# Kernel optimization log

Hardware: AMD Instinct MI355X
Metric: run time of the kernel (lower is better)

Reference implementation:

```python
import jax, jax.numpy as jnp
import numpy as np

N_NODES = 100000
N_EDGES = 3200000
N_GRAPHS = 4096
BN_EPS = 1e-5


def setup_inputs() -> dict:
    key = jax.random.key(0)
    ks = iter(jax.random.split(key, 64))
    d = {}
    d["x"] = jax.random.normal(next(ks), (N_NODES, 36), dtype=jnp.float32)
    d["edge_index"] = jax.random.randint(next(ks), (2, N_EDGES), 0, N_NODES, dtype=jnp.int32)
    d["batch"] = jnp.sort(jax.random.randint(next(ks), (N_NODES,), 0, N_GRAPHS, dtype=jnp.int32))
    d["num_graphs"] = N_GRAPHS
    # GCN layers: (in, out) per hidden_dims=[128,128,64]
    dims = [(36, 128), (128, 128), (128, 64)]
    for i, (di, do) in enumerate(dims):
        d[f"w{i}"] = jax.random.normal(next(ks), (di, do), dtype=jnp.float32) * (1.0 / np.sqrt(di))
        d[f"b{i}"] = jax.random.normal(next(ks), (do,), dtype=jnp.float32) * 0.01
        d[f"g{i}"] = jax.random.uniform(next(ks), (do,), dtype=jnp.float32, minval=0.5, maxval=1.5)
        d[f"be{i}"] = jax.random.normal(next(ks), (do,), dtype=jnp.float32) * 0.01
        d[f"m{i}"] = jax.random.normal(next(ks), (do,), dtype=jnp.float32) * 0.01
        d[f"v{i}"] = jax.random.uniform(next(ks), (do,), dtype=jnp.float32, minval=0.5, maxval=1.5)
    # FC head: 64 -> 128 -> 64 -> 2
    d["fw0"] = jax.random.normal(next(ks), (64, 128), dtype=jnp.float32) * (1.0 / 8.0)
    d["fb0"] = jax.random.normal(next(ks), (128,), dtype=jnp.float32) * 0.01
    d["fw1"] = jax.random.normal(next(ks), (128, 64), dtype=jnp.float32) * (1.0 / np.sqrt(128))
    d["fb1"] = jax.random.normal(next(ks), (64,), dtype=jnp.float32) * 0.01
    d["ow"] = jax.random.normal(next(ks), (64, 2), dtype=jnp.float32) * (1.0 / 8.0)
    d["ob"] = jax.random.normal(next(ks), (2,), dtype=jnp.float32) * 0.01
    return d


def _gcn_layer(x, w, b, src, dst, norm_e, norm_self, n_nodes):
    # PyG GCNConv with self-loops: out[i] = sum_j norm_ij * (x_j @ W) + b
    xw = x @ w                                   # [N, out]
    msg = xw[src] * norm_e[:, None]              # gather + scale, [E, out]
    agg = jax.ops.segment_sum(msg, dst, num_segments=n_nodes)
    return agg + xw * norm_self[:, None] + b     # self-loop contribution + bias


def _bn_eval(x, g, be, m, v):
    return g * (x - m) * jax.lax.rsqrt(v + BN_EPS) + be


def reference(x, edge_index, batch, num_graphs,
              w0, b0, g0, be0, m0, v0,
              w1, b1, g1, be1, m1, v1,
              w2, b2, g2, be2, m2, v2,
              fw0, fb0, fw1, fb1, ow, ob):
    n = x.shape[0]
    src, dst = edge_index[0], edge_index[1]
    # symmetric GCN normalization with self-loops (gcn_norm)
    deg = jax.ops.segment_sum(jnp.ones(src.shape[0], x.dtype), dst, num_segments=n) + 1.0
    dinv = jax.lax.rsqrt(deg)
    norm_e = dinv[src] * dinv[dst]   # per-edge coeff
    norm_self = dinv * dinv          # self-loop coeff = 1/deg

    params = [(w0, b0, g0, be0, m0, v0), (w1, b1, g1, be1, m1, v1), (w2, b2, g2, be2, m2, v2)]
    h = x
    for (w, b, g, be, m, v) in params:
        h = _gcn_layer(h, w, b, src, dst, norm_e, norm_self, n)
        h = jax.nn.relu(_bn_eval(h, g, be, m, v))  # dropout inactive in eval

    # global mean pool over graphs
    sums = jax.ops.segment_sum(h, batch, num_segments=num_graphs)          # [G, 64]
    cnt = jax.ops.segment_sum(jnp.ones(n, h.dtype), batch, num_segments=num_graphs)
    pooled = sums / jnp.maximum(cnt, 1.0)[:, None]

    h = jax.nn.relu(pooled @ fw0 + fb0)
    h = jax.nn.relu(h @ fw1 + fb1)
    return h @ ow + ob
```

## Files before the change

kernel.cpp:

```cpp
#include <hip/hip_runtime.h>
#include <hip/hip_fp16.h>

#define BN_EPS 1e-5f

#define BUCK_SHIFT 9
#define NBUCK_MAX 256
#define BCAP 20480
#define PBLK 512

__global__ __launch_bounds__(256) void fused_scatter(const int* __restrict__ src,
                                                     const int* __restrict__ dst,
                                                     int* __restrict__ gcnt,
                                                     int2* __restrict__ ebuf,
                                                     int nE, int nbuck, int chunk) {
    __shared__ int h[NBUCK_MAX], rbase[NBUCK_MAX], cur[NBUCK_MAX];
    const int blk = blockIdx.x, tid = threadIdx.x;
    for (int j = tid; j < nbuck; j += 256) { h[j] = 0; cur[j] = 0; }
    __syncthreads();
    const int base = blk * chunk;
    const int end = min(base + chunk, nE);
    for (int i = base + tid; i < end; i += 256)
        atomicAdd(&h[dst[i] >> BUCK_SHIFT], 1);
    __syncthreads();
    for (int j = tid; j < nbuck; j += 256)
        rbase[j] = h[j] ? atomicAdd(&gcnt[j], h[j]) : 0;
    __syncthreads();
    for (int i = base + tid; i < end; i += 256) {
        int s = src[i], d = dst[i];
        int b = d >> BUCK_SHIFT;
        int p = rbase[b] + atomicAdd(&cur[b], 1);
        if (p < BCAP) ebuf[(size_t)b * BCAP + p] = make_int2(s, d);
    }
}

__global__ __launch_bounds__(256) void fused_csr(const int2* __restrict__ ebuf,
                                                 const int* __restrict__ gcnt,
                                                 const float* __restrict__ x,
                                                 const int* __restrict__ batch,
                                                 int* __restrict__ degI,
                                                 float* __restrict__ dinv,
                                                 int* __restrict__ row_start,
                                                 int* __restrict__ src_sorted,
                                                 __half* __restrict__ xs_h,
                                                 float* __restrict__ cnt, int n) {
    __shared__ int deg[512];
    __shared__ int cur[512];
    __shared__ float sdi[512];
    __shared__ int tmp[256];
    __shared__ int s_low_total;
    const int b = blockIdx.x, tid = threadIdx.x;
    const int nb = b << BUCK_SHIFT;
    const int cntb = min(gcnt[b], BCAP);
    const int2* __restrict__ eb = ebuf + (size_t)b * BCAP;

    for (int j = tid; j < 512; j += 256) deg[j] = 0;
    __syncthreads();
    for (int i = tid; i < cntb; i += 256)
        atomicAdd(&deg[eb[i].y - nb], 1);
    __syncthreads();

    for (int j = tid; j < 512; j += 256) {
        int node = nb + j;
        if (node < n) {
            int d = deg[j];
            degI[node] = d;
            float di = rsqrtf((float)d + 1.0f);
            dinv[node] = di;
            sdi[j] = di;
        }
    }

    int v0 = deg[tid];
    tmp[tid] = v0;
    __syncthreads();
    for (int off = 1; off < 256; off <<= 1) {
        int t = (tid >= off) ? tmp[tid - off] : 0;
        __syncthreads();
        tmp[tid] += t;
        __syncthreads();
    }
    int ex_low = tmp[tid] - v0;
    if (tid == 255) s_low_total = tmp[255];
    __syncthreads();
    int low_total = s_low_total;
    int v1 = deg[256 + tid];
    __syncthreads();
    tmp[tid] = v1;
    __syncthreads();
    for (int off = 1; off < 256; off <<= 1) {
        int t = (tid >= off) ? tmp[tid - off] : 0;
        __syncthreads();
        tmp[tid] += t;
        __syncthreads();
    }
    int ex_high = tmp[tid] - v1 + low_total;

    const int gbase = b * BCAP;
    if (nb + tid < n) row_start[nb + tid] = gbase + ex_low;
    if (nb + 256 + tid < n) row_start[nb + 256 + tid] = gbase + ex_high;
    cur[tid] = ex_low;
    cur[256 + tid] = ex_high;
    __syncthreads();

    for (int i = tid; i < cntb; i += 256) {
        int2 ed = eb[i];
        int p = atomicAdd(&cur[ed.y - nb], 1);
        src_sorted[gbase + p] = ed.x;
    }

    for (int idx = tid; idx < 512 * 18; idx += 256) {
        int j = idx / 18;
        int node = nb + j;
        if (node < n) {
            int c = idx - j * 18;
            float2 v = *(const float2*)(x + (size_t)node * 36 + 2 * c);
            float di = sdi[j];
            *(__half2*)(xs_h + (size_t)node * 36 + 2 * c) = __floats2half2_rn(v.x * di, v.y * di);
        }
    }

    for (int j = tid; j < 512; j += 256) {
        int node = nb + j;
        if (node < n) unsafeAtomicAdd(&cnt[batch[node]], 1.0f);
    }
}

__global__ __launch_bounds__(256) void agg_pull36w_h(const __half* __restrict__ xs_h,
                                                     const int* __restrict__ row_start,
                                                     const int* __restrict__ degI,
                                                     const int* __restrict__ src_sorted,
                                                     const float* __restrict__ dinv,
                                                     __half* __restrict__ out, int n) {
    int node = __builtin_amdgcn_readfirstlane((int)(blockIdx.x * 4 + (threadIdx.x >> 6)));
    if (node >= n) return;
    const int lane = threadIdx.x & 63;
    int e = row_start[node];
    const int re = e + degI[node];
    const float di = dinv[node];

    const char* __restrict__ xb = (const char*)xs_h;
    const unsigned loff = (unsigned)lane << 2;

    float2 acc = make_float2(0.f, 0.f);
    if (lane < 18) acc = __half22float2(*(const __half2*)(xb + ((unsigned)node * 72u + loff)));

    for (; e + 3 < re; e += 4) {
        int s0 = src_sorted[e], s1 = src_sorted[e + 1],
            s2 = src_sorted[e + 2], s3 = src_sorted[e + 3];
        if (lane < 18) {
            float2 a0 = __half22float2(*(const __half2*)(xb + ((unsigned)s0 * 72u + loff)));
            float2 a1 = __half22float2(*(const __half2*)(xb + ((unsigned)s1 * 72u + loff)));
            float2 a2 = __half22float2(*(const __half2*)(xb + ((unsigned)s2 * 72u + loff)));
            float2 a3 = __half22float2(*(const __half2*)(xb + ((unsigned)s3 * 72u + loff)));
            acc.x += (a0.x + a1.x) + (a2.x + a3.x);
            acc.y += (a0.y + a1.y) + (a2.y + a3.y);
        }
    }
    for (; e < re; e++) {
        int s = src_sorted[e];
        if (lane < 18) {
            float2 a = __half22float2(*(const __half2*)(xb + ((unsigned)s * 72u + loff)));
            acc.x += a.x;
            acc.y += a.y;
        }
    }
    if (lane < 18) {
        __half2 o = __floats2half2_rn(acc.x * di, acc.y * di);
        *(__half2*)((char*)out + ((unsigned)node * 72u + loff)) = o;
    }
}

__global__ __launch_bounds__(256) void agg_pull_wave2_h(const __half* __restrict__ feat_h,
                                                        const int* __restrict__ row_start,
                                                        const int* __restrict__ degI,
                                                        const int* __restrict__ src_sorted,
                                                        const float* __restrict__ dinv,
                                                        __half* __restrict__ out, int n) {
    int node = __builtin_amdgcn_readfirstlane((int)(blockIdx.x * 4 + (threadIdx.x >> 6)));
    if (node >= n) return;
    const int lane = threadIdx.x & 63;
    int e = row_start[node];
    const int re = e + degI[node];
    const float di = dinv[node];

    const char* __restrict__ fb = (const char*)feat_h;
    const unsigned loff = (unsigned)lane << 2;

    float2 acc = __half22float2(*(const __half2*)(fb + (((unsigned)node << 8) + loff)));

    for (; e + 3 < re; e += 4) {
        int s0 = src_sorted[e], s1 = src_sorted[e + 1],
            s2 = src_sorted[e + 2], s3 = src_sorted[e + 3];
        float2 a0 = __half22float2(*(const __half2*)(fb + (((unsigned)s0 << 8) + loff)));
        float2 a1 = __half22float2(*(const __half2*)(fb + (((unsigned)s1 << 8) + loff)));
        float2 a2 = __half22float2(*(const __half2*)(fb + (((unsigned)s2 << 8) + loff)));
        float2 a3 = __half22float2(*(const __half2*)(fb + (((unsigned)s3 << 8) + loff)));
        acc.x += (a0.x + a1.x) + (a2.x + a3.x);
        acc.y += (a0.y + a1.y) + (a2.y + a3.y);
    }
    for (; e < re; e++) {
        int s = src_sorted[e];
        float2 a = __half22float2(*(const __half2*)(fb + (((unsigned)s << 8) + loff)));
        acc.x += a.x;
        acc.y += a.y;
    }
    __half2 o = __floats2half2_rn(acc.x * di, acc.y * di);
    *(__half2*)((char*)out + (((unsigned)node << 8) + loff)) = o;
}

template<int IN, int OUT, bool BNRELU, bool SCALEOUT>
__global__ __launch_bounds__(256) void gemm_rth(const __half* __restrict__ in,
                                                const float* __restrict__ W,
                                                const float* __restrict__ bias,
                                                const float* __restrict__ gg,
                                                const float* __restrict__ bb,
                                                const float* __restrict__ mm,
                                                const float* __restrict__ vv,
                                                const float* __restrict__ dscale,
                                                __half* __restrict__ out, int n) {
    constexpr int BM = 64;
    constexpr int TN = 8;
    constexpr int CG = OUT / TN;
    constexpr int RG = 256 / CG;
    constexpr int TM = BM / RG;
    constexpr int PAD = (IN == 36) ? 8 : 4;
    constexpr int LDW = IN + PAD;
    __shared__ float s_a[BM][LDW];

    const int r0 = blockIdx.x * BM;
    const int tid = threadIdx.x;

    if constexpr (IN == 128) {
        for (int i8 = tid; i8 < BM * 16; i8 += 256) {
            int idx = i8 * 8;
            int r = idx >> 7;
            int k = idx & 127;
            int row = r0 + r;
            uint4 v = make_uint4(0u, 0u, 0u, 0u);
            if (row < n) v = *(const uint4*)(in + (size_t)row * 128 + k);
            const __half2* hp = (const __half2*)&v;
            float2 f0 = __half22float2(hp[0]);
            float2 f1 = __half22float2(hp[1]);
            float2 f2 = __half22float2(hp[2]);
            float2 f3 = __half22float2(hp[3]);
            *(float4*)&s_a[r][k]     = make_float4(f0.x, f0.y, f1.x, f1.y);
            *(float4*)&s_a[r][k + 4] = make_float4(f2.x, f2.y, f3.x, f3.y);
        }
    } else {
        for (int i2 = tid; i2 < BM * (IN / 2); i2 += 256) {
            int r = i2 / (IN / 2);
            int k = (i2 - r * (IN / 2)) * 2;
            int row = r0 + r;
            __half2 hv;
            *(unsigned*)&hv = 0u;
            if (row < n) hv = *(const __half2*)(in + (size_t)row * IN + k);
            float2 f = __half22float2(hv);
            s_a[r][k] = f.x;
            s_a[r][k + 1] = f.y;
        }
    }
    __syncthreads();

    const int tx = tid % CG;
    const int ty = tid / CG;
    const int c0 = tx * TN;
    const int rr = ty * TM;

    float acc[TM][TN];
#pragma unroll
    for (int j = 0; j < TM; j++)
#pragma unroll
        for (int t = 0; t < TN; t++) acc[j][t] = 0.0f;

#pragma unroll 2
    for (int k = 0; k < IN; k += 4) {
        float4 a[TM];
#pragma unroll
        for (int j = 0; j < TM; j++) a[j] = *(const float4*)&s_a[rr + j][k];
#pragma unroll
        for (int kk = 0; kk < 4; kk++) {
            float4 wv0 = *(const float4*)(W + (size_t)(k + kk) * OUT + c0);
            float4 wv1 = *(const float4*)(W + (size_t)(k + kk) * OUT + c0 + 4);
#pragma unroll
            for (int j = 0; j < TM; j++) {
                float av = (kk == 0) ? a[j].x : (kk == 1) ? a[j].y : (kk == 2) ? a[j].z : a[j].w;
                acc[j][0] += av * wv0.x;
                acc[j][1] += av * wv0.y;
                acc[j][2] += av * wv0.z;
                acc[j][3] += av * wv0.w;
                acc[j][4] += av * wv1.x;
                acc[j][5] += av * wv1.y;
                acc[j][6] += av * wv1.z;
                acc[j][7] += av * wv1.w;
            }
        }
    }

    float scl[TN], sft[TN];
    if constexpr (BNRELU) {
#pragma unroll
        for (int t = 0; t < TN; t++) {
            float s = gg[c0 + t] * rsqrtf(vv[c0 + t] + BN_EPS);
            scl[t] = s;
            sft[t] = bb[c0 + t] + (bias[c0 + t] - mm[c0 + t]) * s;
        }
    }

#pragma unroll
    for (int j = 0; j < TM; j++) {
        int row = r0 + rr + j;
        if (row < n) {
            float ds = 1.0f;
            if constexpr (SCALEOUT) ds = dscale[row];
            union { __half h[8]; uint4 v; } u;
#pragma unroll
            for (int t = 0; t < TN; t++) {
                float val = acc[j][t];
                if constexpr (BNRELU) val = fmaxf(val * scl[t] + sft[t], 0.0f);
                if constexpr (SCALEOUT) val *= ds;
                u.h[t] = __float2half_rn(val);
            }
            *(uint4*)(out + (size_t)row * OUT + c0) = u.v;
        }
    }
}

__global__ __launch_bounds__(256) void agg_pull_pool_h(const __half* __restrict__ feat_h,
                                                       const int* __restrict__ row_start,
                                                       const int* __restrict__ degI,
                                                       const int* __restrict__ src_sorted,
                                                       const float* __restrict__ dinv,
                                                       const float* __restrict__ bias,
                                                       const float* __restrict__ gg,
                                                       const float* __restrict__ bb,
                                                       const float* __restrict__ mm,
                                                       const float* __restrict__ vv,
                                                       const int* __restrict__ batch,
                                                       float* __restrict__ pool, int n) {
    int node = __builtin_amdgcn_readfirstlane((int)(blockIdx.x * 4 + (threadIdx.x >> 6)));
    if (node >= n) return;
    const int lane = threadIdx.x & 63;
    int e = row_start[node];
    const int re = e + degI[node];
    const float di = dinv[node];

    const char* __restrict__ fb = (const char*)feat_h;
    const unsigned loff = (unsigned)lane << 1;

    float acc = __half2float(*(const __half*)(fb + (((unsigned)node << 7) + loff)));

    for (; e + 3 < re; e += 4) {
        int s0 = src_sorted[e], s1 = src_sorted[e + 1],
            s2 = src_sorted[e + 2], s3 = src_sorted[e + 3];
        float a0 = __half2float(*(const __half*)(fb + (((unsigned)s0 << 7) + loff)));
        float a1 = __half2float(*(const __half*)(fb + (((unsigned)s1 << 7) + loff)));
        float a2 = __half2float(*(const __half*)(fb + (((unsigned)s2 << 7) + loff)));
        float a3 = __half2float(*(const __half*)(fb + (((unsigned)s3 << 7) + loff)));
        acc += (a0 + a1) + (a2 + a3);
    }
    for (; e < re; e++) {
        acc += __half2float(*(const __half*)(fb + (((unsigned)src_sorted[e] << 7) + loff)));
    }
    float h = acc * di + bias[lane];
    float scale = gg[lane] * rsqrtf(vv[lane] + BN_EPS);
    float val = fmaxf((h - mm[lane]) * scale + bb[lane], 0.0f);
    unsafeAtomicAdd(&pool[(size_t)batch[node] * 64 + lane], val);
}

__global__ __launch_bounds__(128) void fc_head_kernel(const float* __restrict__ pool,
                                                      const float* __restrict__ cnt,
                                                      const float* __restrict__ fw0,
                                                      const float* __restrict__ fb0,
                                                      const float* __restrict__ fw1,
                                                      const float* __restrict__ fb1,
                                                      const float* __restrict__ ow,
                                                      const float* __restrict__ ob,
                                                      float* __restrict__ out) {
    int g = blockIdx.x, tid = threadIdx.x;
    __shared__ float p[64], h1[128], h2[64];
    if (tid < 64) p[tid] = pool[g * 64 + tid] / fmaxf(cnt[g], 1.0f);
    __syncthreads();
    {
        float acc = fb0[tid];
        for (int k = 0; k < 64; k++) acc += p[k] * fw0[k * 128 + tid];
        h1[tid] = fmaxf(acc, 0.0f);
    }
    __syncthreads();
    if (tid < 64) {
        float acc = fb1[tid];
        for (int k = 0; k < 128; k++) acc += h1[k] * fw1[k * 64 + tid];
        h2[tid] = fmaxf(acc, 0.0f);
    }
    __syncthreads();
    if (tid < 2) {
        float acc = ob[tid];
        for (int k = 0; k < 64; k++) acc += h2[k] * ow[k * 2 + tid];
        out[g * 2 + tid] = acc;
    }
}

extern "C" void kernel_launch(void* const* d_in, const int* in_sizes, int n_in,
                              void* d_out, int out_size, void* d_ws, size_t ws_size,
                              hipStream_t stream) {
    const float* x     = (const float*)d_in[0];
    const int*   eidx  = (const int*)d_in[1];
    const int*   batch = (const int*)d_in[2];
    const float* w0 = (const float*)d_in[4];
    const float* b0 = (const float*)d_in[5];
    const float* g0 = (const float*)d_in[6];
    const float* be0 = (const float*)d_in[7];
    const float* m0 = (const float*)d_in[8];
    const float* v0 = (const float*)d_in[9];
    const float* w1 = (const float*)d_in[10];
    const float* b1 = (const float*)d_in[11];
    const float* g1 = (const float*)d_in[12];
    const float* be1 = (const float*)d_in[13];
    const float* m1 = (const float*)d_in[14];
    const float* v1 = (const float*)d_in[15];
    const float* w2 = (const float*)d_in[16];
    const float* b2 = (const float*)d_in[17];
    const float* g2 = (const float*)d_in[18];
    const float* be2 = (const float*)d_in[19];
    const float* m2 = (const float*)d_in[20];
    const float* v2 = (const float*)d_in[21];
    const float* fw0 = (const float*)d_in[22];
    const float* fb0 = (const float*)d_in[23];
    const float* fw1 = (const float*)d_in[24];
    const float* fb1 = (const float*)d_in[25];
    const float* ow = (const float*)d_in[26];
    const float* ob = (const float*)d_in[27];

    const int N = in_sizes[0] / 36;
    const int E = in_sizes[1] / 2;
    const int G = out_size / 2;
    const int* src = eidx;
    const int* dst = eidx + E;

    const int nbuck = (N + 511) >> BUCK_SHIFT;
    const int chunk = (E + PBLK - 1) / PBLK;

    char* wsb = (char*)d_ws;
    int2*   ebuf       = (int2*)wsb;    wsb += (size_t)nbuck * BCAP * 8;
    __half* F1         = (__half*)wsb;  wsb += (size_t)N * 128 * 2;
    __half* F1a        = (__half*)wsb;  wsb += (size_t)N * 128 * 2;
    __half* F2         = (__half*)wsb;  wsb += (size_t)N * 64 * 2;
    __half* A36h       = (__half*)wsb;  wsb += (size_t)N * 36 * 2;
    __half* xs_h       = (__half*)wsb;  wsb += (size_t)N * 36 * 2;
    int*    src_sorted = (int*)wsb;     wsb += (size_t)nbuck * BCAP * 4;
    int*    degI       = (int*)wsb;     wsb += (size_t)N * 4;
    int*    row_start  = (int*)wsb;     wsb += (size_t)N * 4;
    float*  dinv       = (float*)wsb;   wsb += (size_t)N * 4;
    float*  pool       = (float*)wsb;   wsb += (size_t)G * 64 * 4;
    float*  cnt        = (float*)wsb;   wsb += (size_t)G * 4;
    int*    gcnt       = (int*)wsb;     wsb += 256 * 4;
    __half* F1b        = (__half*)ebuf;

    hipMemsetAsync(gcnt, 0, 256 * 4, stream);
    hipMemsetAsync(pool, 0, (size_t)G * 64 * 4, stream);
    hipMemsetAsync(cnt, 0, (size_t)G * 4, stream);

    fused_scatter<<<PBLK, 256, 0, stream>>>(src, dst, gcnt, ebuf, E, nbuck, chunk);
    fused_csr<<<nbuck, 256, 0, stream>>>(ebuf, gcnt, x, batch, degI, dinv, row_start,
                                         src_sorted, xs_h, cnt, N);

    const int NW = (N + 3) / 4;
    const int NG = (N + 63) / 64;

    agg_pull36w_h<<<NW, 256, 0, stream>>>(xs_h, row_start, degI, src_sorted, dinv, A36h, N);
    gemm_rth<36, 128, true, true><<<NG, 256, 0, stream>>>(
        A36h, w0, b0, g0, be0, m0, v0, dinv, F1, N);

    agg_pull_wave2_h<<<NW, 256, 0, stream>>>(F1, row_start, degI, src_sorted, dinv, F1a, N);
    gemm_rth<128, 128, true, false><<<NG, 256, 0, stream>>>(
        F1a, w1, b1, g1, be1, m1, v1, nullptr, F1b, N);

    gemm_rth<128, 64, false, true><<<NG, 256, 0, stream>>>(
        F1b, w2, nullptr, nullptr, nullptr, nullptr, nullptr, dinv, F2, N);

    agg_pull_pool_h<<<NW, 256, 0, stream>>>(
        F2, row_start, degI, src_sorted, dinv, b2, g2, be2, m2, v2, batch, pool, N);

    fc_head_kernel<<<G, 128, 0, stream>>>(pool, cnt, fw0, fb0, fw1, fb1, ow, ob, (float*)d_out);
}
```

Measured before the change: 670.1 us.

## Replace scalar FP32 GEMMs with MFMA f16 kernels using repacked weights

Replaces the shared-memory scalar FMA GEMM kernels for all three GCN layers with MFMA 16x16x32 f16 kernels. Weights are converted to half and laid out per lane by a small repack kernel each call. The layer-0 aggregation output is padded from 36 to 64 columns so K fits the MFMA shape, and row buffers are padded to a multiple of 64. Weights now run in half precision, and the 36-wide path relies on the padding lanes (18..31) writing zero accumulators.

```diff
diff --git a/kernel.cpp b/kernel.cpp
--- a/kernel.cpp
+++ b/kernel.cpp
@@ -7,6 +7,9 @@
 #define NBUCK_MAX 256
 #define BCAP 20480
 #define PBLK 512
+
+typedef _Float16 f16x8 __attribute__((ext_vector_type(8)));
+typedef float f32x4 __attribute__((ext_vector_type(4)));
 
 __global__ __launch_bounds__(256) void fused_scatter(const int* __restrict__ src,
                                                      const int* __restrict__ dst,
@@ -125,6 +128,96 @@
     }
 }
 
+__global__ __launch_bounds__(256) void repack_w(const float* __restrict__ w0,
+                                                const float* __restrict__ w1,
+                                                const float* __restrict__ w2,
+                                                __half* __restrict__ Wp0,
+                                                __half* __restrict__ Wp1,
+                                                __half* __restrict__ Wp2) {
+    const int tid = threadIdx.x;
+    if (blockIdx.x == 0) {
+        for (int idx = tid; idx < 8 * 4 * 64 * 8; idx += 256) {
+            int j = idx & 7, lane = (idx >> 3) & 63, kb = (idx >> 9) & 3, nt = idx >> 11;
+            int k = kb * 32 + (lane >> 4) * 8 + j, c = nt * 16 + (lane & 15);
+            Wp1[idx] = __float2half_rn(w1[k * 128 + c]);
+        }
+    } else if (blockIdx.x == 1) {
+        for (int idx = tid; idx < 4 * 4 * 64 * 8; idx += 256) {
+            int j = idx & 7, lane = (idx >> 3) & 63, kb = (idx >> 9) & 3, nt = idx >> 11;
+            int k = kb * 32 + (lane >> 4) * 8 + j, c = nt * 16 + (lane & 15);
+            Wp2[idx] = __float2half_rn(w2[k * 64 + c]);
+        }
+    } else {
+        for (int idx = tid; idx < 8 * 2 * 64 * 8; idx += 256) {
+            int j = idx & 7, lane = (idx >> 3) & 63, kb = (idx >> 9) & 1, nt = idx >> 10;
+            int k = kb * 32 + (lane >> 4) * 8 + j, c = nt * 16 + (lane & 15);
+            Wp0[idx] = (k < 36) ? __float2half_rn(w0[k * 128 + c]) : __float2half_rn(0.0f);
+        }
+    }
+}
+
+template<int LDK, int KB, int OUT, int NT, bool BNRELU, bool SCALEOUT>
+__global__ __launch_bounds__(256) void gemm_mfma(const __half* __restrict__ in,
+                                                 const __half* __restrict__ Wp,
+                                                 const float* __restrict__ bias,
+                                                 const float* __restrict__ gg,
+                                                 const float* __restrict__ bb,
+                                                 const float* __restrict__ mm,
+                                                 const float* __restrict__ vv,
+                                                 const float* __restrict__ dscale,
+                                                 __half* __restrict__ out, int n) {
+    const int lane = threadIdx.x & 63;
+    const int wave = threadIdx.x >> 6;
+    const int r0 = blockIdx.x * 64 + wave * 16;
+    const int arow = r0 + (lane & 15);
+    const int kg = lane >> 4;
+
+    f16x8 a[KB];
+#pragma unroll
+    for (int kb = 0; kb < KB; kb++)
+        a[kb] = *(const f16x8*)(in + (size_t)arow * LDK + kb * 32 + kg * 8);
+
+    f32x4 acc[NT];
+#pragma unroll
+    for (int nt = 0; nt < NT; nt++) {
+        f32x4 z = {0.0f, 0.0f, 0.0f, 0.0f};
+        acc[nt] = z;
+    }
+
+#pragma unroll
+    for (int nt = 0; nt < NT; nt++) {
+#pragma unroll
+        for (int kb = 0; kb < KB; kb++) {
+            f16x8 b = *(const f16x8*)(Wp + ((size_t)(nt * KB + kb) * 64 + lane) * 8);
+            acc[nt] = __builtin_amdgcn_mfma_f32_16x16x32_f16(a[kb], b, acc[nt], 0, 0, 0);
+        }
+    }
+
+    const int col = lane & 15;
+    const int rbase = r0 + kg * 4;
+    float ds[4] = {1.f, 1.f, 1.f, 1.f};
+    if constexpr (SCALEOUT) {
+#pragma unroll
+        for (int r = 0; r < 4; r++) ds[r] = dscale[rbase + r];
+    }
+#pragma unroll
+    for (int nt = 0; nt < NT; nt++) {
+        const int c = nt * 16 + col;
+        float s = 1.f, t = 0.f;
+        if constexpr (BNRELU) {
+            s = gg[c] * rsqrtf(vv[c] + BN_EPS);
+            t = bb[c] + (bias[c] - mm[c]) * s;
+        }
+#pragma unroll
+        for (int r = 0; r < 4; r++) {
+            float val = acc[nt][r];
+            if constexpr (BNRELU) val = fmaxf(val * s + t, 0.0f);
+            if constexpr (SCALEOUT) val *= ds[r];
+            out[(size_t)(rbase + r) * OUT + c] = __float2half_rn(val);
+        }
+    }
+}
+
 __global__ __launch_bounds__(256) void agg_pull36w_h(const __half* __restrict__ xs_h,
                                                      const int* __restrict__ row_start,
                                                      const int* __restrict__ degI,
@@ -164,9 +257,9 @@
             acc.y += a.y;
         }
     }
-    if (lane < 18) {
+    if (lane < 32) {
         __half2 o = __floats2half2_rn(acc.x * di, acc.y * di);
-        *(__half2*)((char*)out + ((unsigned)node * 72u + loff)) = o;
+        *(__half2*)((char*)out + (((unsigned)node << 7) + loff)) = o;
     }
 }
 
@@ -206,123 +299,6 @@
     }
     __half2 o = __floats2half2_rn(acc.x * di, acc.y * di);
     *(__half2*)((char*)out + (((unsigned)node << 8) + loff)) = o;
-}
-
-template<int IN, int OUT, bool BNRELU, bool SCALEOUT>
-__global__ __launch_bounds__(256) void gemm_rth(const __half* __restrict__ in,
-                                                const float* __restrict__ W,
-                                                const float* __restrict__ bias,
-                                                const float* __restrict__ gg,
-                                                const float* __restrict__ bb,
-                                                const float* __restrict__ mm,
-                                                const float* __restrict__ vv,
-                                                const float* __restrict__ dscale,
-                                                __half* __restrict__ out, int n) {
-    constexpr int BM = 64;
-    constexpr int TN = 8;
-    constexpr int CG = OUT / TN;
-    constexpr int RG = 256 / CG;
-    constexpr int TM = BM / RG;
-    constexpr int PAD = (IN == 36) ? 8 : 4;
-    constexpr int LDW = IN + PAD;
-    __shared__ float s_a[BM][LDW];
-
-    const int r0 = blockIdx.x * BM;
-    const int tid = threadIdx.x;
-
-    if constexpr (IN == 128) {
-        for (int i8 = tid; i8 < BM * 16; i8 += 256) {
-            int idx = i8 * 8;
-            int r = idx >> 7;
-            int k = idx & 127;
-            int row = r0 + r;
-            uint4 v = make_uint4(0u, 0u, 0u, 0u);
-            if (row < n) v = *(const uint4*)(in + (size_t)row * 128 + k);
-            const __half2* hp = (const __half2*)&v;
-            float2 f0 = __half22float2(hp[0]);
-            float2 f1 = __half22float2(hp[1]);
-            float2 f2 = __half22float2(hp[2]);
-            float2 f3 = __half22float2(hp[3]);
-            *(float4*)&s_a[r][k]     = make_float4(f0.x, f0.y, f1.x, f1.y);
-            *(float4*)&s_a[r][k + 4] = make_float4(f2.x, f2.y, f3.x, f3.y);
-        }
-    } else {
-        for (int i2 = tid; i2 < BM * (IN / 2); i2 += 256) {
-            int r = i2 / (IN / 2);
-            int k = (i2 - r * (IN / 2)) * 2;
-            int row = r0 + r;
-            __half2 hv;
-            *(unsigned*)&hv = 0u;
-            if (row < n) hv = *(const __half2*)(in + (size_t)row * IN + k);
-            float2 f = __half22float2(hv);
-            s_a[r][k] = f.x;
-            s_a[r][k + 1] = f.y;
-        }
-    }
-    __syncthreads();
-
-    const int tx = tid % CG;
-    const int ty = tid / CG;
-    const int c0 = tx * TN;
-    const int rr = ty * TM;
-
-    float acc[TM][TN];
-#pragma unroll
-    for (int j = 0; j < TM; j++)
-#pragma unroll
-        for (int t = 0; t < TN; t++) acc[j][t] = 0.0f;
-
-#pragma unroll 2
-    for (int k = 0; k < IN; k += 4) {
-        float4 a[TM];
-#pragma unroll
-        for (int j = 0; j < TM; j++) a[j] = *(const float4*)&s_a[rr + j][k];
-#pragma unroll
-        for (int kk = 0; kk < 4; kk++) {
-            float4 wv0 = *(const float4*)(W + (size_t)(k + kk) * OUT + c0);
-            float4 wv1 = *(const float4*)(W + (size_t)(k + kk) * OUT + c0 + 4);
-#pragma unroll
-            for (int j = 0; j < TM; j++) {
-                float av = (kk == 0) ? a[j].x : (kk == 1) ? a[j].y : (kk == 2) ? a[j].z : a[j].w;
-                acc[j][0] += av * wv0.x;
-                acc[j][1] += av * wv0.y;
-                acc[j][2] += av * wv0.z;
-                acc[j][3] += av * wv0.w;
-                acc[j][4] += av * wv1.x;
-                acc[j][5] += av * wv1.y;
-                acc[j][6] += av * wv1.z;
-                acc[j][7] += av * wv1.w;
-            }
-        }
-    }
-
-    float scl[TN], sft[TN];
-    if constexpr (BNRELU) {
-#pragma unroll
-        for (int t = 0; t < TN; t++) {
-            float s = gg[c0 + t] * rsqrtf(vv[c0 + t] + BN_EPS);
-            scl[t] = s;
-            sft[t] = bb[c0 + t] + (bias[c0 + t] - mm[c0 + t]) * s;
-        }
-    }
-
-#pragma unroll
-    for (int j = 0; j < TM; j++) {
-        int row = r0 + rr + j;
-        if (row < n) {
-            float ds = 1.0f;
-            if constexpr (SCALEOUT) ds = dscale[row];
-            union { __half h[8]; uint4 v; } u;
-#pragma unroll
-            for (int t = 0; t < TN; t++) {
-                float val = acc[j][t];
-                if constexpr (BNRELU) val = fmaxf(val * scl[t] + sft[t], 0.0f);
-                if constexpr (SCALEOUT) val *= ds;
-                u.h[t] = __float2half_rn(val);
-            }
-            *(uint4*)(out + (size_t)row * OUT + c0) = u.v;
-        }
-    }
 }
 
 __global__ __launch_bounds__(256) void agg_pull_pool_h(const __half* __restrict__ feat_h,
@@ -438,44 +414,49 @@
 
     const int nbuck = (N + 511) >> BUCK_SHIFT;
     const int chunk = (E + PBLK - 1) / PBLK;
+    const int NPAD = ((N + 63) / 64) * 64;
+    const int NGP = NPAD / 64;
 
     char* wsb = (char*)d_ws;
     int2*   ebuf       = (int2*)wsb;    wsb += (size_t)nbuck * BCAP * 8;
-    __half* F1         = (__half*)wsb;  wsb += (size_t)N * 128 * 2;
-    __half* F1a        = (__half*)wsb;  wsb += (size_t)N * 128 * 2;
-    __half* F2         = (__half*)wsb;  wsb += (size_t)N * 64 * 2;
-    __half* A36h       = (__half*)wsb;  wsb += (size_t)N * 36 * 2;
+    __half* F1         = (__half*)wsb;  wsb += (size_t)NPAD * 128 * 2;
+    __half* F1a        = (__half*)wsb;  wsb += (size_t)NPAD * 128 * 2;
+    __half* F2         = (__half*)wsb;  wsb += (size_t)NPAD * 64 * 2;
+    __half* A36h       = (__half*)wsb;  wsb += (size_t)NPAD * 64 * 2;
     __half* xs_h       = (__half*)wsb;  wsb += (size_t)N * 36 * 2;
     int*    src_sorted = (int*)wsb;     wsb += (size_t)nbuck * BCAP * 4;
     int*    degI       = (int*)wsb;     wsb += (size_t)N * 4;
     int*    row_start  = (int*)wsb;     wsb += (size_t)N * 4;
-    float*  dinv       = (float*)wsb;   wsb += (size_t)N * 4;
+    float*  dinv       = (float*)wsb;   wsb += (size_t)NPAD * 4;
     float*  pool       = (float*)wsb;   wsb += (size_t)G * 64 * 4;
     float*  cnt        = (float*)wsb;   wsb += (size_t)G * 4;
     int*    gcnt       = (int*)wsb;     wsb += 256 * 4;
+    __half* Wp0        = (__half*)wsb;  wsb += 8192 * 2;
+    __half* Wp1        = (__half*)wsb;  wsb += 16384 * 2;
+    __half* Wp2        = (__half*)wsb;  wsb += 8192 * 2;
     __half* F1b        = (__half*)ebuf;
 
     hipMemsetAsync(gcnt, 0, 256 * 4, stream);
     hipMemsetAsync(pool, 0, (size_t)G * 64 * 4, stream);
     hipMemsetAsync(cnt, 0, (size_t)G * 4, stream);
+    repack_w<<<3, 256, 0, stream>>>(w0, w1, w2, Wp0, Wp1, Wp2);
 
     fused_scatter<<<PBLK, 256, 0, stream>>>(src, dst, gcnt, ebuf, E, nbuck, chunk);
     fused_csr<<<nbuck, 256, 0, stream>>>(ebuf, gcnt, x, batch, degI, dinv, row_start,
                                          src_sorted, xs_h, cnt, N);
 
     const int NW = (N + 3) / 4;
-    const int NG = (N + 63) / 64;
 
     agg_pull36w_h<<<NW, 256, 0, stream>>>(xs_h, row_start, degI, src_sorted, dinv, A36h, N);
-    gemm_rth<36, 128, true, true><<<NG, 256, 0, stream>>>(
-        A36h, w0, b0, g0, be0, m0, v0, dinv, F1, N);
+    gemm_mfma<64, 2, 128, 8, true, true><<<NGP, 256, 0, stream>>>(
+        A36h, Wp0, b0, g0, be0, m0, v0, dinv, F1, N);
 
     agg_pull_wave2_h<<<NW, 256, 0, stream>>>(F1, row_start, degI, src_sorted, dinv, F1a, N);
-    gemm_rth<128, 128, true, false><<<NG, 256, 0, stream>>>(
-        F1a, w1, b1, g1, be1, m1, v1, nullptr, F1b, N);
-
-    gemm_rth<128, 64, false, true><<<NG, 256, 0, stream>>>(
-        F1b, w2, nullptr, nullptr, nullptr, nullptr, nullptr, dinv, F2, N);
+    gemm_mfma<128, 4, 128, 8, true, false><<<NGP, 256, 0, stream>>>(
+        F1a, Wp1, b1, g1, be1, m1, v1, nullptr, F1b, N);
+
+    gemm_mfma<128, 4, 64, 4, false, true><<<NGP, 256, 0, stream>>>(
+        F1b, Wp2, nullptr, nullptr, nullptr, nullptr, nullptr, dinv, F2, N);
 
     agg_pull_pool_h<<<NW, 256, 0, stream>>>(
         F2, row_start, degI, src_sorted, dinv, b2, g2, be2, m2, v2, batch, pool, N);
```

Result: faster. 576.5 us (-14.0%).
